# Kernel tuning notes

Measured on AMD Instinct MI355X. Metric: run time of the kernel, lower is better.

The kernel has to match this reference:

```python
import jax, jax.numpy as jnp
import numpy as np

NUM_NODES = 16384
EMBED_DIM = 128
BATCH = 32


def setup_inputs() -> dict:
    key = jax.random.key(0)
    k1, k2, k3 = jax.random.split(key, 3)
    # xavier_uniform for embed_node: bound = sqrt(6/(fan_in+fan_out))
    xb = float(np.sqrt(6.0 / (NUM_NODES + EMBED_DIM)))
    embed_node = jax.random.uniform(k1, (NUM_NODES, EMBED_DIM), minval=-xb, maxval=xb, dtype=jnp.float32)
    # nn.Linear default init: U(-1/sqrt(fan_in), 1/sqrt(fan_in)). These params exist but
    # provably do not affect the output (root node at depth 0 is never updated).
    lb = float(np.sqrt(1.0 / EMBED_DIM))
    W_self = jax.random.uniform(k2, (EMBED_DIM, EMBED_DIM), minval=-lb, maxval=lb, dtype=jnp.float32)
    W_child = jax.random.uniform(k3, (EMBED_DIM, EMBED_DIM), minval=-lb, maxval=lb, dtype=jnp.float32)
    return {"embed_node": embed_node, "W_self": W_self, "W_child": W_child, "batch_size": BATCH}


def reference(embed_node, W_self, W_child, batch_size):
    # Faithful math of TreeBasedSpatialEmbedding.forward:
    # - adj_matrix_path=None -> tree_structures is None -> node_emb = embed_node.
    # - (Even with trees: depth-0 root is skipped in _tree_aggregate, so
    #   root_embedding[root_node] == embed_node[root_node]; identical result.)
    # Then: unsqueeze(0).expand(B,-1,-1) -> [B,N,D]; transpose(1,2) -> [B,D,N]; unsqueeze(-1) -> [B,D,N,1]
    n, d = embed_node.shape
    out = jnp.broadcast_to(embed_node.T[None, :, :], (batch_size, d, n))[..., None]
    return out
```

## Files before the change

### kernel.cpp

```cpp
#include <hip/hip_runtime.h>
#include <hip/hip_bf16.h>


#define NN 16384
#define DD 128
#define NT 64
#define BT 4
#define NBATCH 32

__global__ __launch_bounds__(256) void tree_embed_bcast_kernel(
    const float* __restrict__ E, float* __restrict__ out) {
    __shared__ float lds[DD][NT + 1];

    const int n0 = blockIdx.x * NT;
    const int b0 = blockIdx.y * BT;
    const int tid = threadIdx.x;

    {
        const int c = tid & 31;
        const int r = tid >> 5;
        #pragma unroll
        for (int it = 0; it < NT / 8; ++it) {
            const int n = r + it * 8;
            const float4 v = *reinterpret_cast<const float4*>(
                &E[(size_t)(n0 + n) * DD + (c << 2)]);
            lds[(c << 2) + 0][n] = v.x;
            lds[(c << 2) + 1][n] = v.y;
            lds[(c << 2) + 2][n] = v.z;
            lds[(c << 2) + 3][n] = v.w;
        }
    }
    __syncthreads();

    const int j = tid & 15;
    const int row0 = tid >> 4;
    #pragma unroll 4
    for (int it = 0; it < (BT * DD) / 16; ++it) {
        const int row = row0 + it * 16;
        const int d = row & (DD - 1);
        const int b = b0 + (row >> 7);
        float4 v;
        v.x = lds[d][(j << 2) + 0];
        v.y = lds[d][(j << 2) + 1];
        v.z = lds[d][(j << 2) + 2];
        v.w = lds[d][(j << 2) + 3];
        const size_t oidx = (((size_t)b * DD + d) * NN) + n0 + (j << 2);
        *reinterpret_cast<float4*>(&out[oidx]) = v;
    }
}

extern "C" void kernel_launch(void* const* d_in, const int* in_sizes, int n_in,
                              void* d_out, int out_size, void* d_ws, size_t ws_size,
                              hipStream_t stream) {
    const float* E = (const float*)d_in[0];
    float* out = (float*)d_out;
    dim3 grid(NN / NT, NBATCH / BT);
    dim3 block(256);
    hipLaunchKernelGGL(tree_embed_bcast_kernel, grid, block, 0, stream, E, out);
}
```

Baseline: 47.91 us.

## Split into transpose of batch 0 then streaming copy to remaining batches

Transposes the embedding once into batch slot 0 of the output, then launches a second kernel that copies that slab to the other 31 batch slots using nontemporal vector stores. This replaces the per-batch LDS transpose with a plain streaming copy. In exchange it adds a second launch and reads 31 copies of the 8 MB slab back from memory, or from cache if it stays resident, instead of reading only the small input.

```diff
diff --git a/kernel.cpp b/kernel.cpp
--- a/kernel.cpp
+++ b/kernel.cpp
@@ -5,15 +5,15 @@
 #define NN 16384
 #define DD 128
 #define NT 64
-#define BT 4
 #define NBATCH 32
 
-__global__ __launch_bounds__(256) void tree_embed_bcast_kernel(
+typedef float f4_t __attribute__((ext_vector_type(4)));
+
+__global__ __launch_bounds__(256) void transpose_b0_kernel(
     const float* __restrict__ E, float* __restrict__ out) {
     __shared__ float lds[DD][NT + 1];
 
     const int n0 = blockIdx.x * NT;
-    const int b0 = blockIdx.y * BT;
     const int tid = threadIdx.x;
 
     {
@@ -22,7 +22,7 @@
         #pragma unroll
         for (int it = 0; it < NT / 8; ++it) {
             const int n = r + it * 8;
-            const float4 v = *reinterpret_cast<const float4*>(
+            const f4_t v = *reinterpret_cast<const f4_t*>(
                 &E[(size_t)(n0 + n) * DD + (c << 2)]);
             lds[(c << 2) + 0][n] = v.x;
             lds[(c << 2) + 1][n] = v.y;
@@ -34,18 +34,32 @@
 
     const int j = tid & 15;
     const int row0 = tid >> 4;
-    #pragma unroll 4
-    for (int it = 0; it < (BT * DD) / 16; ++it) {
-        const int row = row0 + it * 16;
-        const int d = row & (DD - 1);
-        const int b = b0 + (row >> 7);
-        float4 v;
+    #pragma unroll
+    for (int it = 0; it < DD / 16; ++it) {
+        const int d = row0 + it * 16;
+        f4_t v;
         v.x = lds[d][(j << 2) + 0];
         v.y = lds[d][(j << 2) + 1];
         v.z = lds[d][(j << 2) + 2];
         v.w = lds[d][(j << 2) + 3];
-        const size_t oidx = (((size_t)b * DD + d) * NN) + n0 + (j << 2);
-        *reinterpret_cast<float4*>(&out[oidx]) = v;
+        *reinterpret_cast<f4_t*>(&out[(size_t)d * NN + n0 + (j << 2)]) = v;
+    }
+}
+
+__global__ __launch_bounds__(256) void bcast_kernel(
+    const float* __restrict__ src, float* __restrict__ out) {
+    const size_t BSZ = (size_t)DD * NN;
+    const size_t CHUNK = BSZ / 64;
+    const size_t base = (size_t)blockIdx.y * CHUNK;
+    const float* __restrict__ s = src + base;
+    float* __restrict__ dst = out + (size_t)(blockIdx.x + 1) * BSZ + base;
+    const int tid = threadIdx.x;
+
+    #pragma unroll 8
+    for (int it = 0; it < 32; ++it) {
+        const size_t idx = (size_t)(it * 256 + tid) << 2;
+        const f4_t v = *reinterpret_cast<const f4_t*>(&s[idx]);
+        __builtin_nontemporal_store(v, reinterpret_cast<f4_t*>(&dst[idx]));
     }
 }
 
@@ -54,7 +68,9 @@
                               hipStream_t stream) {
     const float* E = (const float*)d_in[0];
     float* out = (float*)d_out;
-    dim3 grid(NN / NT, NBATCH / BT);
-    dim3 block(256);
-    hipLaunchKernelGGL(tree_embed_bcast_kernel, grid, block, 0, stream, E, out);
+
+    hipLaunchKernelGGL(transpose_b0_kernel, dim3(NN / NT), dim3(256), 0, stream,
+                       E, out);
+    hipLaunchKernelGGL(bcast_kernel, dim3(NBATCH - 1, 64), dim3(256), 0, stream,
+                       out, out);
 }
```

Measured after the change: 60.49 us. 1.26x slower.

## Drop LDS transpose; gather strided columns and broadcast registers to all batches

Applied to the files above, without the earlier changes.

Replaces the shared-memory tiled transpose with a per-thread strided gather: each block handles one embedding dimension and a 2048-node chunk, loading eight scalar values into registers. Each thread then writes those two float4 vectors to all 32 batch copies. This removes the LDS traffic and barrier and reuses each loaded value across every batch. The cost is uncoalesced input reads with a 512-byte stride, which may rely on L2 since each input cache line is touched by many blocks.

```diff
diff --git a/kernel.cpp b/kernel.cpp
--- a/kernel.cpp
+++ b/kernel.cpp
@@ -4,48 +4,30 @@
 
 #define NN 16384
 #define DD 128
-#define NT 64
-#define BT 4
-#define NBATCH 32
+#define NB 32
+#define CHUNK 2048
+
+typedef float f4_t __attribute__((ext_vector_type(4)));
 
 __global__ __launch_bounds__(256) void tree_embed_bcast_kernel(
     const float* __restrict__ E, float* __restrict__ out) {
-    __shared__ float lds[DD][NT + 1];
+    const int d  = blockIdx.x;
+    const int n0 = blockIdx.y * CHUNK;
+    const int t  = threadIdx.x;
 
-    const int n0 = blockIdx.x * NT;
-    const int b0 = blockIdx.y * BT;
-    const int tid = threadIdx.x;
+    const float* e0 = E + (size_t)(n0 + (t << 2)) * DD + d;
+    const float* e1 = e0 + (size_t)1024 * DD;
+    f4_t va, vb;
+    va.x = e0[0 * DD]; va.y = e0[1 * DD]; va.z = e0[2 * DD]; va.w = e0[3 * DD];
+    vb.x = e1[0 * DD]; vb.y = e1[1 * DD]; vb.z = e1[2 * DD]; vb.w = e1[3 * DD];
 
-    {
-        const int c = tid & 31;
-        const int r = tid >> 5;
-        #pragma unroll
-        for (int it = 0; it < NT / 8; ++it) {
-            const int n = r + it * 8;
-            const float4 v = *reinterpret_cast<const float4*>(
-                &E[(size_t)(n0 + n) * DD + (c << 2)]);
-            lds[(c << 2) + 0][n] = v.x;
-            lds[(c << 2) + 1][n] = v.y;
-            lds[(c << 2) + 2][n] = v.z;
-            lds[(c << 2) + 3][n] = v.w;
-        }
-    }
-    __syncthreads();
-
-    const int j = tid & 15;
-    const int row0 = tid >> 4;
-    #pragma unroll 4
-    for (int it = 0; it < (BT * DD) / 16; ++it) {
-        const int row = row0 + it * 16;
-        const int d = row & (DD - 1);
-        const int b = b0 + (row >> 7);
-        float4 v;
-        v.x = lds[d][(j << 2) + 0];
-        v.y = lds[d][(j << 2) + 1];
-        v.z = lds[d][(j << 2) + 2];
-        v.w = lds[d][(j << 2) + 3];
-        const size_t oidx = (((size_t)b * DD + d) * NN) + n0 + (j << 2);
-        *reinterpret_cast<float4*>(&out[oidx]) = v;
+    float* o = out + (size_t)d * NN + n0 + (t << 2);
+    const size_t BSTRIDE = (size_t)DD * NN;
+    #pragma unroll
+    for (int b = 0; b < NB; ++b) {
+        float* p = o + (size_t)b * BSTRIDE;
+        *reinterpret_cast<f4_t*>(p) = va;
+        *reinterpret_cast<f4_t*>(p + 1024) = vb;
     }
 }
 
@@ -54,7 +36,7 @@
                               hipStream_t stream) {
     const float* E = (const float*)d_in[0];
     float* out = (float*)d_out;
-    dim3 grid(NN / NT, NBATCH / BT);
-    dim3 block(256);
-    hipLaunchKernelGGL(tree_embed_bcast_kernel, grid, block, 0, stream, E, out);
+    dim3 grid(DD, NN / CHUNK);
+    hipLaunchKernelGGL(tree_embed_bcast_kernel, grid, dim3(256), 0, stream,
+                       E, out);
 }
```

Measured after the change: 55.63 us. +16.1%, slower.
